# Kernel tuning notes

Measured on AMD Instinct MI355X. Metric: run time of the kernel, lower is better.

The kernel has to match this reference:

```python
import jax, jax.numpy as jnp
import numpy as np

REG = 1e-6

def maxpool2(x):  # NCHW, kernel 2 stride 2
    return jax.lax.reduce_window(x, -jnp.inf, jax.lax.max, (1, 1, 2, 2), (1, 1, 2, 2), 'VALID')

def conv2d_same(x, w, b):  # NCHW / OIHW, stride 1, padding 1 (3x3)
    y = jax.lax.conv_general_dilated(x, w, (1, 1), ((1, 1), (1, 1)),
                                     dimension_numbers=('NCHW', 'OIHW', 'NCHW'))
    return y + b[None, :, None, None]

def batch_skew(a):  # [B,3] -> [B,3,3]
    z = jnp.zeros_like(a[:, 0])
    return jnp.stack([
        jnp.stack([z, -a[:, 2], a[:, 1]], -1),
        jnp.stack([a[:, 2], z, -a[:, 0]], -1),
        jnp.stack([-a[:, 1], a[:, 0], z], -1)], 1)

def batch_twist2mat(w):  # Rodrigues: so(3) -> SO(3)
    theta = jnp.maximum(jnp.linalg.norm(w, axis=1, keepdims=True), 1e-12)  # [B,1]
    A = batch_skew(w / theta)
    s = jnp.sin(theta)[:, :, None]
    c = (1.0 - jnp.cos(theta))[:, :, None]
    return jnp.eye(3, dtype=w.dtype) + s * A + c * (A @ A)

def setup_inputs() -> dict:
    key = jax.random.key(0)
    ks = jax.random.split(key, 24)
    B, C, H, W = 64, 8, 240, 320
    HW = H * W
    A = jax.random.normal(ks[0], (B, 6, 6), jnp.float32)
    JtJ = A @ jnp.swapaxes(A, 1, 2) + 6.0 * jnp.eye(6, dtype=jnp.float32)  # SPD Hessian
    inp = {
        'JtJ': JtJ,
        'Jt': jax.random.normal(ks[1], (B, 6, HW), jnp.float32),
        'weights': jax.random.uniform(ks[2], (B, 1, H, W), jnp.float32),
        'R': jax.random.normal(ks[3], (B, 1, H, W), jnp.float32),
        'pose_R': jax.random.normal(ks[4], (B, 3, 3), jnp.float32),
        'pose_t': jax.random.normal(ks[5], (B, 3, 1), jnp.float32),
        'invD0': jax.random.uniform(ks[6], (B, 1, H, W), jnp.float32),
        'invD1': jax.random.uniform(ks[7], (B, 1, H, W), jnp.float32),
        'x0': jax.random.normal(ks[8], (B, C, H, W), jnp.float32),
        'x1': jax.random.normal(ks[9], (B, C, H, W), jnp.float32),
        'K': jax.random.normal(ks[10], (B, 3, 3), jnp.float32),
        # DampingNet parameters
        'consts': jax.random.normal(ks[11], (6, 6), jnp.float32),
        'conv1_w': jax.random.normal(ks[12], (8, 1, 3, 3), jnp.float32) * 0.2,
        'conv1_b': jnp.zeros((8,), jnp.float32),
        'conv2_w': jax.random.normal(ks[13], (16, 8, 3, 3), jnp.float32) * 0.1,
        'conv2_b': jnp.zeros((16,), jnp.float32),
        'fc1_w': jax.random.normal(ks[14], (64, 19200), jnp.float32) * 0.01,
        'fc1_b': jnp.zeros((64,), jnp.float32),
        'fc2_w': jax.random.normal(ks[15], (6, 64), jnp.float32) * 0.1,
        'fc2_b': jnp.zeros((6,), jnp.float32),
    }
    return inp

def dampingnet(R, consts, c1w, c1b, c2w, c2b, f1w, f1b, f2w, f2b):
    B = R.shape[0]
    h = maxpool2(R)
    h = jax.nn.relu(conv2d_same(h, c1w, c1b))
    h = maxpool2(h)
    h = jax.nn.relu(conv2d_same(h, c2w, c2b))
    h = maxpool2(h)
    h = h.reshape(B, -1)  # [B, 19200], NCHW flatten matches torch
    h = jax.nn.relu(h @ f1w.T + f1b)
    lambdas_w = jax.nn.softmax(h @ f2w.T + f2b, axis=-1)  # [B,6]
    wc = lambdas_w @ consts  # [B,6]
    min_, max_ = -6.0, -5.0
    return 10.0 ** (min_ + jax.nn.sigmoid(wc) * (max_ - min_))  # [B,6]

def reference(JtJ, Jt, weights, R, pose_R, pose_t, invD0, invD1, x0, x1, K,
              consts, conv1_w, conv1_b, conv2_w, conv2_b, fc1_w, fc1_b, fc2_w, fc2_b):
    B = JtJ.shape[0]
    wR = (weights * R).reshape(B, -1, 1)            # [B,HW,1]
    JtR = Jt @ wR                                   # [B,6,1]
    lam = dampingnet(R, consts, conv1_w, conv1_b, conv2_w, conv2_b,
                     fc1_w, fc1_b, fc2_w, fc2_b)    # [B,6]
    trace = jnp.trace(JtJ, axis1=1, axis2=2)        # [B]
    diag_add = lam + 1e-6 * trace[:, None]          # [B,6]
    eye6 = jnp.eye(6, dtype=JtJ.dtype)
    Hessian = JtJ + diag_add[:, :, None] * eye6     # diag_mask*lambda + epsilon
    # inverse_update_pose: regularized batched 6x6 inverse
    Hinv = jnp.linalg.inv(Hessian + REG * eye6)
    xi = Hinv @ JtR                                 # [B,6,1]
    d_R = batch_twist2mat(-xi[:, :3, 0])            # [B,3,3]
    d_t = -(d_R @ xi[:, 3:])                        # [B,3,1]
    R_new = pose_R @ d_R
    t_new = pose_R @ d_t + pose_t
    return jnp.concatenate([R_new, t_new], axis=2)  # [B,3,4] pose (R|t)
```

## Files before the change

### kernel.cpp

```cpp
#include <hip/hip_runtime.h>
#include <math.h>

#define BATCH 64
#define WW 320
#define HWTOT 76800
#define HW4 19200
#define NJTRB 512
#define JSL4 2400
#define NCONV1 1280
#define KS 64
#define NSLICE 300

__global__ __launch_bounds__(256) void k_front(
    const float* __restrict__ Jt, const float* __restrict__ wgt,
    const float* __restrict__ Rin, const float* __restrict__ c1w,
    const float* __restrict__ c1b, float* __restrict__ part,
    float* __restrict__ h1) {
  __shared__ float smem[34 * 37 + 96];
  int tid = threadIdx.x;
  if (blockIdx.x < NJTRB) {
    int b = blockIdx.x >> 3, s = blockIdx.x & 7;
    const float4* w4 = (const float4*)(wgt + (size_t)b * HWTOT);
    const float4* r4 = (const float4*)(Rin + (size_t)b * HWTOT);
    const float4* j4 = (const float4*)(Jt + (size_t)b * 6 * HWTOT);
    int base = s * JSL4;
    float acc[6] = {0.f, 0.f, 0.f, 0.f, 0.f, 0.f};
#pragma unroll 3
    for (int k = 0; k < 9; ++k) {
      int t = base + k * 256 + tid;
      float4 wv = w4[t], rv = r4[t];
      float4 p;
      p.x = wv.x * rv.x; p.y = wv.y * rv.y; p.z = wv.z * rv.z; p.w = wv.w * rv.w;
#pragma unroll
      for (int i = 0; i < 6; ++i) {
        float4 jv = j4[i * HW4 + t];
        acc[i] += jv.x * p.x + jv.y * p.y + jv.z * p.z + jv.w * p.w;
      }
    }
    if (tid < 96) {
      int t = base + 2304 + tid;
      float4 wv = w4[t], rv = r4[t];
      float4 p;
      p.x = wv.x * rv.x; p.y = wv.y * rv.y; p.z = wv.z * rv.z; p.w = wv.w * rv.w;
#pragma unroll
      for (int i = 0; i < 6; ++i) {
        float4 jv = j4[i * HW4 + t];
        acc[i] += jv.x * p.x + jv.y * p.y + jv.z * p.z + jv.w * p.w;
      }
    }
#pragma unroll
    for (int i = 0; i < 6; ++i) {
      float v = acc[i];
      for (int off = 32; off; off >>= 1) v += __shfl_down(v, off, 64);
      acc[i] = v;
    }
    float* sred = smem;
    int lane = tid & 63, wid = tid >> 6;
    if (lane == 0) {
#pragma unroll
      for (int i = 0; i < 6; ++i) sred[wid * 6 + i] = acc[i];
    }
    __syncthreads();
    if (tid < 6) {
      part[blockIdx.x * 6 + tid] =
          sred[0 + tid] + sred[6 + tid] + sred[12 + tid] + sred[18 + tid];
    }
    return;
  }
  int cb = blockIdx.x - NJTRB;
  int b = cb / 20, rem = cb % 20;
  int by = rem / 5, bx = rem % 5;
  float (*sA)[37] = (float(*)[37])smem;
  float* sW = smem + 34 * 37;
  float* sB = sW + 72;
  if (tid < 72) sW[tid] = c1w[(tid & 7) * 9 + (tid >> 3)];
  if (tid < 8) sB[tid] = c1b[tid];
  int iy0 = 32 * by - 1;
  const float* src = Rin + (size_t)b * HWTOT;
  for (int idx = tid; idx < 34 * 18; idx += 256) {
    int pr = idx / 18, c4 = idx % 18;
    int py = iy0 + pr;
    int gx = 64 * bx - 4 + 4 * c4;
    float cell0 = 0.f, cell1 = 0.f;
    if (py >= 0 && py < 120 && gx >= 0 && gx < 320) {
      const float4* row0 = (const float4*)(src + (size_t)(2 * py) * WW + gx);
      const float4* row1 = (const float4*)(src + (size_t)(2 * py + 1) * WW + gx);
      float4 v0 = row0[0], v1 = row1[0];
      cell0 = fmaxf(fmaxf(v0.x, v0.y), fmaxf(v1.x, v1.y));
      cell1 = fmaxf(fmaxf(v0.z, v0.w), fmaxf(v1.z, v1.w));
    }
    sA[pr][2 * c4] = cell0;
    sA[pr][2 * c4 + 1] = cell1;
  }
  __syncthreads();
  int ly = tid / 16, lx = tid % 16;
  int y = 16 * by + ly, x = 16 * bx + lx;
  float win[16];
#pragma unroll
  for (int r = 0; r < 4; ++r)
#pragma unroll
    for (int c = 0; c < 4; ++c) win[r * 4 + c] = sA[2 * ly + r][2 * lx + c + 1];
  float acc[8][4];
#pragma unroll
  for (int oc = 0; oc < 8; ++oc)
#pragma unroll
    for (int p = 0; p < 4; ++p) acc[oc][p] = 0.f;
#pragma unroll
  for (int tap = 0; tap < 9; ++tap) {
    int ky = tap / 3, kx = tap % 3;
#pragma unroll
    for (int oc = 0; oc < 8; ++oc) {
      float wv = sW[tap * 8 + oc];
#pragma unroll
      for (int py = 0; py < 2; ++py)
#pragma unroll
        for (int px = 0; px < 2; ++px)
          acc[oc][py * 2 + px] += wv * win[(py + ky) * 4 + (px + kx)];
    }
  }
  if (y < 60) {
    float v[8];
#pragma unroll
    for (int oc = 0; oc < 8; ++oc)
      v[oc] = fmaxf(fmaxf(fmaxf(acc[oc][0], acc[oc][1]), fmaxf(acc[oc][2], acc[oc][3])) + sB[oc], 0.f);
    float4* dst = (float4*)(h1 + (((size_t)b * 60 + y) * 80 + x) * 8);
    dst[0] = make_float4(v[0], v[1], v[2], v[3]);
    dst[1] = make_float4(v[4], v[5], v[6], v[7]);
  }
}

__global__ __launch_bounds__(256) void k_conv2(
    const float* __restrict__ h1, const float* __restrict__ c2w,
    const float* __restrict__ c2b, float* __restrict__ h2) {
  __shared__ float sA[8][34][38];
  int b = blockIdx.z >> 1, ocg = blockIdx.z & 1;
  int ty0 = blockIdx.y * 16, tx0 = blockIdx.x * 16;
  int tid = threadIdx.x;
  int iy0 = ty0 * 2 - 1, ix0 = tx0 * 2 - 1;
  const float* src = h1 + (size_t)b * 60 * 80 * 8;
  for (int idx = tid; idx < 34 * 34; idx += 256) {
    int r = idx / 34, c = idx % 34;
    int gy = iy0 + r, gx = ix0 + c;
    float4 v0 = make_float4(0.f, 0.f, 0.f, 0.f), v1 = v0;
    if (gy >= 0 && gy < 60 && gx >= 0 && gx < 80) {
      const float4* p = (const float4*)(src + ((size_t)gy * 80 + gx) * 8);
      v0 = p[0]; v1 = p[1];
    }
    sA[0][r][c] = v0.x; sA[1][r][c] = v0.y; sA[2][r][c] = v0.z; sA[3][r][c] = v0.w;
    sA[4][r][c] = v1.x; sA[5][r][c] = v1.y; sA[6][r][c] = v1.z; sA[7][r][c] = v1.w;
  }
  __syncthreads();
  int ly = tid / 16, lx = tid % 16;
  float acc[8][4];
#pragma unroll
  for (int o = 0; o < 8; ++o)
#pragma unroll
    for (int p = 0; p < 4; ++p) acc[o][p] = 0.f;
  const float* wbase = c2w + ocg * 8 * 72;
#pragma unroll
  for (int ic = 0; ic < 8; ++ic) {
    float win[16];
#pragma unroll
    for (int r = 0; r < 4; ++r)
#pragma unroll
      for (int c = 0; c < 4; ++c) win[r * 4 + c] = sA[ic][2 * ly + r][2 * lx + c];
#pragma unroll
    for (int tap = 0; tap < 9; ++tap) {
      int ky = tap / 3, kx = tap % 3;
#pragma unroll
      for (int o = 0; o < 8; ++o) {
        float wv = wbase[o * 72 + ic * 9 + tap];
#pragma unroll
        for (int py = 0; py < 2; ++py)
#pragma unroll
          for (int px = 0; px < 2; ++px)
            acc[o][py * 2 + px] += wv * win[(py + ky) * 4 + (px + kx)];
      }
    }
  }
  int y = ty0 + ly, x = tx0 + lx;
  if (y < 30 && x < 40) {
#pragma unroll
    for (int o = 0; o < 8; ++o) {
      int oc = ocg * 8 + o;
      float m = fmaxf(fmaxf(acc[o][0], acc[o][1]), fmaxf(acc[o][2], acc[o][3])) + c2b[oc];
      h2[(((size_t)b * 16 + oc) * 30 + y) * 40 + x] = fmaxf(m, 0.f);
    }
  }
}

__global__ __launch_bounds__(256) void k_fc1_part(
    const float* __restrict__ h2, const float* __restrict__ f1w,
    float* __restrict__ fcpart) {
  __shared__ __align__(16) float sH[KS * 68];
  __shared__ __align__(16) float sWt[KS * 68];
  int sl = blockIdx.x, k0 = sl * KS;
  int tid = threadIdx.x;
  for (int idx = tid; idx < 64 * KS; idx += 256) {
    int b = idx >> 6, kk = idx & 63;
    sH[kk * 68 + b] = h2[(size_t)b * 19200 + k0 + kk];
    sWt[kk * 68 + b] = f1w[(size_t)b * 19200 + k0 + kk];
  }
  __syncthreads();
  int bq = tid & 15, jq = tid >> 4;
  int b0 = bq * 4, j0 = jq * 4;
  float acc[4][4];
#pragma unroll
  for (int i = 0; i < 4; ++i)
#pragma unroll
    for (int j = 0; j < 4; ++j) acc[i][j] = 0.f;
  for (int kk = 0; kk < KS; ++kk) {
    float4 hv = *(const float4*)&sH[kk * 68 + b0];
    float4 wv = *(const float4*)&sWt[kk * 68 + j0];
    float hb[4] = {hv.x, hv.y, hv.z, hv.w};
    float wb[4] = {wv.x, wv.y, wv.z, wv.w};
#pragma unroll
    for (int i = 0; i < 4; ++i)
#pragma unroll
      for (int j = 0; j < 4; ++j) acc[i][j] += hb[i] * wb[j];
  }
#pragma unroll
  for (int i = 0; i < 4; ++i)
#pragma unroll
    for (int j = 0; j < 4; ++j)
      fcpart[(size_t)(b0 + i) * 19200 + sl * 64 + (j0 + j)] = acc[i][j];
}

__global__ __launch_bounds__(256) void k_final(
    const float* __restrict__ fcpart, const float* __restrict__ f1b,
    const float* __restrict__ f2w, const float* __restrict__ f2b,
    const float* __restrict__ consts, const float* __restrict__ part,
    const float* __restrict__ JtJ, const float* __restrict__ poseR,
    const float* __restrict__ poseT, float* __restrict__ out) {
  __shared__ __align__(16) float sred[16 * 64];
  __shared__ float fc1v[64];
  __shared__ float sf2w[384];
  __shared__ float sf2b[8];
  __shared__ float sconst[36];
  __shared__ float lg[6];
  __shared__ float lamv[6];
  __shared__ float jtrv[6];
  int b = blockIdx.x, tid = threadIdx.x;
  for (int i = tid; i < 384; i += 256) sf2w[i] = f2w[i];
  if (tid < 6) sf2b[tid] = f2b[tid];
  if (tid < 36) sconst[tid] = consts[tid];
  {
    const float4* fp4 = (const float4*)(fcpart + (size_t)b * 19200);
    int sg = tid >> 4, j4 = tid & 15;
    float4 a = make_float4(0.f, 0.f, 0.f, 0.f);
    for (int s = sg; s < NSLICE; s += 16) {
      float4 v = fp4[s * 16 + j4];
      a.x += v.x; a.y += v.y; a.z += v.z; a.w += v.w;
    }
    ((float4*)sred)[sg * 16 + j4] = a;
  }
  if (tid >= 64 && tid < 70) {
    int i = tid - 64;
    float v = 0.f;
    for (int s = 0; s < 8; ++s) v += part[(b * 8 + s) * 6 + i];
    jtrv[i] = v;
  }
  __syncthreads();
  if (tid < 64) {
    float v = 0.f;
#pragma unroll
    for (int sg = 0; sg < 16; ++sg) v += sred[sg * 64 + tid];
    fc1v[tid] = fmaxf(v + f1b[tid], 0.f);
  }
  __syncthreads();
  if (tid < 6) {
    float v = sf2b[tid];
#pragma unroll
    for (int k = 0; k < 64; ++k) v += fc1v[k] * sf2w[tid * 64 + k];
    lg[tid] = v;
  }
  __syncthreads();
  if (tid < 6) {
    float m = lg[0];
#pragma unroll
    for (int i = 1; i < 6; ++i) m = fmaxf(m, lg[i]);
    float e[6], ssum = 0.f;
#pragma unroll
    for (int i = 0; i < 6; ++i) { e[i] = expf(lg[i] - m); ssum += e[i]; }
    float inv = 1.f / ssum;
    float wc = 0.f;
#pragma unroll
    for (int i = 0; i < 6; ++i) wc += (e[i] * inv) * sconst[i * 6 + tid];
    float sg = 1.f / (1.f + expf(-wc));
    lamv[tid] = expf((-6.f + sg) * 2.302585092994046f);
  }
  __syncthreads();
  if (tid == 0) {
    float Hm[6][6];
    const float* srcH = JtJ + b * 36;
    float tr = 0.f;
#pragma unroll
    for (int i = 0; i < 6; ++i) {
#pragma unroll
      for (int jj = 0; jj < 6; ++jj) Hm[i][jj] = srcH[i * 6 + jj];
      tr += srcH[i * 6 + i];
    }
    float rhs[6];
#pragma unroll
    for (int i = 0; i < 6; ++i) {
      rhs[i] = jtrv[i];
      Hm[i][i] += lamv[i] + 1e-6f * tr + 1e-6f;
    }
    float L[6][6];
#pragma unroll
    for (int i = 0; i < 6; ++i) {
#pragma unroll
      for (int jj = 0; jj < 6; ++jj) {
        if (jj > i) continue;
        float s = Hm[i][jj];
#pragma unroll
        for (int k = 0; k < 6; ++k)
          if (k < jj) s -= L[i][k] * L[jj][k];
        if (i == jj) L[i][jj] = sqrtf(fmaxf(s, 1e-30f));
        else L[i][jj] = s / L[jj][jj];
      }
    }
    float yv[6];
#pragma unroll
    for (int i = 0; i < 6; ++i) {
      float s = rhs[i];
#pragma unroll
      for (int k = 0; k < 6; ++k)
        if (k < i) s -= L[i][k] * yv[k];
      yv[i] = s / L[i][i];
    }
    float xi[6];
#pragma unroll
    for (int ii = 5; ii >= 0; --ii) {
      float s = yv[ii];
#pragma unroll
      for (int k = 0; k < 6; ++k)
        if (k > ii) s -= L[k][ii] * xi[k];
      xi[ii] = s / L[ii][ii];
    }
    float wx = -xi[0], wy = -xi[1], wz = -xi[2];
    float th = fmaxf(sqrtf(wx * wx + wy * wy + wz * wz), 1e-12f);
    float ux = wx / th, uy = wy / th, uz = wz / th;
    float s = sinf(th), c1 = 1.f - cosf(th);
    float Rd[3][3];
    Rd[0][0] = 1.f + c1 * (ux * ux - 1.f);
    Rd[0][1] = -s * uz + c1 * (ux * uy);
    Rd[0][2] = s * uy + c1 * (ux * uz);
    Rd[1][0] = s * uz + c1 * (uy * ux);
    Rd[1][1] = 1.f + c1 * (uy * uy - 1.f);
    Rd[1][2] = -s * ux + c1 * (uy * uz);
    Rd[2][0] = -s * uy + c1 * (uz * ux);
    Rd[2][1] = s * ux + c1 * (uz * uy);
    Rd[2][2] = 1.f + c1 * (uz * uz - 1.f);
    float dt[3];
#pragma unroll
    for (int r = 0; r < 3; ++r)
      dt[r] = -(Rd[r][0] * xi[3] + Rd[r][1] * xi[4] + Rd[r][2] * xi[5]);
    const float* pR = poseR + b * 9;
    const float* pt = poseT + b * 3;
#pragma unroll
    for (int r = 0; r < 3; ++r) {
#pragma unroll
      for (int cc = 0; cc < 3; ++cc) {
        out[b * 12 + r * 4 + cc] =
            pR[r * 3 + 0] * Rd[0][cc] + pR[r * 3 + 1] * Rd[1][cc] + pR[r * 3 + 2] * Rd[2][cc];
      }
      out[b * 12 + r * 4 + 3] =
          pR[r * 3 + 0] * dt[0] + pR[r * 3 + 1] * dt[1] + pR[r * 3 + 2] * dt[2] + pt[r];
    }
  }
}

extern "C" void kernel_launch(void* const* d_in, const int* in_sizes, int n_in,
                              void* d_out, int out_size, void* d_ws, size_t ws_size,
                              hipStream_t stream) {
  const float* JtJ = (const float*)d_in[0];
  const float* Jt = (const float*)d_in[1];
  const float* wts = (const float*)d_in[2];
  const float* Rin = (const float*)d_in[3];
  const float* poseR = (const float*)d_in[4];
  const float* poseT = (const float*)d_in[5];
  const float* consts = (const float*)d_in[11];
  const float* c1w = (const float*)d_in[12];
  const float* c1b = (const float*)d_in[13];
  const float* c2w = (const float*)d_in[14];
  const float* c2b = (const float*)d_in[15];
  const float* f1w = (const float*)d_in[16];
  const float* f1b = (const float*)d_in[17];
  const float* f2w = (const float*)d_in[18];
  const float* f2b = (const float*)d_in[19];
  float* ws = (float*)d_ws;
  float* part = ws;
  float* h1 = part + 3072;
  float* h2 = h1 + 2457600;
  float* fcpart = h2 + 1228800;
  float* out = (float*)d_out;

  k_front<<<dim3(NJTRB + NCONV1), dim3(256), 0, stream>>>(Jt, wts, Rin, c1w, c1b, part, h1);
  k_conv2<<<dim3(3, 2, BATCH * 2), dim3(256), 0, stream>>>(h1, c2w, c2b, h2);
  k_fc1_part<<<dim3(NSLICE), dim3(256), 0, stream>>>(h2, f1w, fcpart);
  k_final<<<dim3(64), dim3(256), 0, stream>>>(fcpart, f1b, f2w, f2b, consts, part,
                                              JtJ, poseR, poseT, out);
}
```

Baseline: 72.10 us.

## Store conv1 activations as fp16 pairs and use fdot2 in conv2

The conv1 output h1 is now written as packed half2 values, which halves its global footprint and the shared-memory staging in conv2. Conv2's weights are packed into half2 pairs once by a block in k_front and staged into shared memory. The inner conv2 loop then uses the fdot2 instruction to handle two input channels per operation instead of scalar fp32 FMAs. This trades activation and weight precision for less memory traffic and fewer ALU instructions.

```diff
diff --git a/kernel.cpp b/kernel.cpp
--- a/kernel.cpp
+++ b/kernel.cpp
@@ -11,11 +11,34 @@
 #define KS 64
 #define NSLICE 300
 
+typedef _Float16 half2_t __attribute__((ext_vector_type(2)));
+union U32H2 { unsigned int u; half2_t h; };
+__device__ __forceinline__ unsigned int pack_h2(float a, float b) {
+  U32H2 x; x.h = half2_t{(_Float16)a, (_Float16)b}; return x.u;
+}
+__device__ __forceinline__ half2_t u_as_h2(unsigned int u) { U32H2 x; x.u = u; return x.h; }
+
+#if defined(__has_builtin)
+#if __has_builtin(__builtin_amdgcn_fdot2)
+#define HAVE_FDOT2 1
+#endif
+#endif
+
+__device__ __forceinline__ float dot2acc(unsigned int a, unsigned int b, float c) {
+#ifdef HAVE_FDOT2
+  return __builtin_amdgcn_fdot2(u_as_h2(a), u_as_h2(b), c, false);
+#else
+  half2_t ah = u_as_h2(a), bh = u_as_h2(b);
+  return c + (float)ah.x * (float)bh.x + (float)ah.y * (float)bh.y;
+#endif
+}
+
 __global__ __launch_bounds__(256) void k_front(
     const float* __restrict__ Jt, const float* __restrict__ wgt,
     const float* __restrict__ Rin, const float* __restrict__ c1w,
-    const float* __restrict__ c1b, float* __restrict__ part,
-    float* __restrict__ h1) {
+    const float* __restrict__ c1b, const float* __restrict__ c2w,
+    float* __restrict__ part, unsigned int* __restrict__ h1u,
+    unsigned int* __restrict__ wpk) {
   __shared__ float smem[34 * 37 + 96];
   int tid = threadIdx.x;
   if (blockIdx.x < NJTRB) {
@@ -70,6 +93,14 @@
   int cb = blockIdx.x - NJTRB;
   int b = cb / 20, rem = cb % 20;
   int by = rem / 5, bx = rem % 5;
+  if (cb == 0) {
+    for (int i = tid; i < 576; i += 256) {
+      int icp = i / 144, tap = (i % 144) / 16, oc = i % 16;
+      float lo = c2w[oc * 72 + (2 * icp) * 9 + tap];
+      float hi = c2w[oc * 72 + (2 * icp + 1) * 9 + tap];
+      wpk[i] = pack_h2(lo, hi);
+    }
+  }
   float (*sA)[37] = (float(*)[37])smem;
   float* sW = smem + 34 * 37;
   float* sB = sW + 72;
@@ -123,31 +154,36 @@
 #pragma unroll
     for (int oc = 0; oc < 8; ++oc)
       v[oc] = fmaxf(fmaxf(fmaxf(acc[oc][0], acc[oc][1]), fmaxf(acc[oc][2], acc[oc][3])) + sB[oc], 0.f);
-    float4* dst = (float4*)(h1 + (((size_t)b * 60 + y) * 80 + x) * 8);
-    dst[0] = make_float4(v[0], v[1], v[2], v[3]);
-    dst[1] = make_float4(v[4], v[5], v[6], v[7]);
+    uint4 st;
+    st.x = pack_h2(v[0], v[1]);
+    st.y = pack_h2(v[2], v[3]);
+    st.z = pack_h2(v[4], v[5]);
+    st.w = pack_h2(v[6], v[7]);
+    *(uint4*)(h1u + (((size_t)b * 60 + y) * 80 + x) * 4) = st;
   }
 }
 
 __global__ __launch_bounds__(256) void k_conv2(
-    const float* __restrict__ h1, const float* __restrict__ c2w,
+    const unsigned int* __restrict__ h1u, const unsigned int* __restrict__ wpk,
     const float* __restrict__ c2b, float* __restrict__ h2) {
-  __shared__ float sA[8][34][38];
+  __shared__ unsigned int sA[4][34][38];
+  __shared__ __align__(16) unsigned int sW[288];
   int b = blockIdx.z >> 1, ocg = blockIdx.z & 1;
   int ty0 = blockIdx.y * 16, tx0 = blockIdx.x * 16;
   int tid = threadIdx.x;
+  for (int i = tid; i < 288; i += 256) {
+    int icp = i / 72, tap = (i % 72) / 8, o = i % 8;
+    sW[i] = wpk[icp * 144 + tap * 16 + ocg * 8 + o];
+  }
   int iy0 = ty0 * 2 - 1, ix0 = tx0 * 2 - 1;
-  const float* src = h1 + (size_t)b * 60 * 80 * 8;
+  const unsigned int* src = h1u + (size_t)b * 60 * 80 * 4;
   for (int idx = tid; idx < 34 * 34; idx += 256) {
     int r = idx / 34, c = idx % 34;
     int gy = iy0 + r, gx = ix0 + c;
-    float4 v0 = make_float4(0.f, 0.f, 0.f, 0.f), v1 = v0;
-    if (gy >= 0 && gy < 60 && gx >= 0 && gx < 80) {
-      const float4* p = (const float4*)(src + ((size_t)gy * 80 + gx) * 8);
-      v0 = p[0]; v1 = p[1];
-    }
-    sA[0][r][c] = v0.x; sA[1][r][c] = v0.y; sA[2][r][c] = v0.z; sA[3][r][c] = v0.w;
-    sA[4][r][c] = v1.x; sA[5][r][c] = v1.y; sA[6][r][c] = v1.z; sA[7][r][c] = v1.w;
+    uint4 v = make_uint4(0u, 0u, 0u, 0u);
+    if (gy >= 0 && gy < 60 && gx >= 0 && gx < 80)
+      v = *(const uint4*)(src + ((size_t)gy * 80 + gx) * 4);
+    sA[0][r][c] = v.x; sA[1][r][c] = v.y; sA[2][r][c] = v.z; sA[3][r][c] = v.w;
   }
   __syncthreads();
   int ly = tid / 16, lx = tid % 16;
@@ -156,25 +192,28 @@
   for (int o = 0; o < 8; ++o)
 #pragma unroll
     for (int p = 0; p < 4; ++p) acc[o][p] = 0.f;
-  const float* wbase = c2w + ocg * 8 * 72;
-#pragma unroll
-  for (int ic = 0; ic < 8; ++ic) {
-    float win[16];
+  const uint4* sW4 = (const uint4*)sW;
+#pragma unroll
+  for (int icp = 0; icp < 4; ++icp) {
+    unsigned int win[16];
 #pragma unroll
     for (int r = 0; r < 4; ++r)
 #pragma unroll
-      for (int c = 0; c < 4; ++c) win[r * 4 + c] = sA[ic][2 * ly + r][2 * lx + c];
+      for (int c = 0; c < 4; ++c) win[r * 4 + c] = sA[icp][2 * ly + r][2 * lx + c];
 #pragma unroll
     for (int tap = 0; tap < 9; ++tap) {
       int ky = tap / 3, kx = tap % 3;
+      uint4 wa = sW4[(icp * 9 + tap) * 2];
+      uint4 wb = sW4[(icp * 9 + tap) * 2 + 1];
+      unsigned int warr[8] = {wa.x, wa.y, wa.z, wa.w, wb.x, wb.y, wb.z, wb.w};
 #pragma unroll
       for (int o = 0; o < 8; ++o) {
-        float wv = wbase[o * 72 + ic * 9 + tap];
 #pragma unroll
         for (int py = 0; py < 2; ++py)
 #pragma unroll
           for (int px = 0; px < 2; ++px)
-            acc[o][py * 2 + px] += wv * win[(py + ky) * 4 + (px + kx)];
+            acc[o][py * 2 + px] =
+                dot2acc(win[(py + ky) * 4 + (px + kx)], warr[o], acc[o][py * 2 + px]);
       }
     }
   }
@@ -391,13 +430,15 @@
   const float* f2b = (const float*)d_in[19];
   float* ws = (float*)d_ws;
   float* part = ws;
-  float* h1 = part + 3072;
-  float* h2 = h1 + 2457600;
+  unsigned int* h1u = (unsigned int*)(ws + 3072);
+  float* h2 = ws + 3072 + 1228800;
   float* fcpart = h2 + 1228800;
+  unsigned int* wpk = (unsigned int*)(fcpart + 1228800);
   float* out = (float*)d_out;
 
-  k_front<<<dim3(NJTRB + NCONV1), dim3(256), 0, stream>>>(Jt, wts, Rin, c1w, c1b, part, h1);
-  k_conv2<<<dim3(3, 2, BATCH * 2), dim3(256), 0, stream>>>(h1, c2w, c2b, h2);
+  k_front<<<dim3(NJTRB + NCONV1), dim3(256), 0, stream>>>(Jt, wts, Rin, c1w, c1b, c2w,
+                                                          part, h1u, wpk);
+  k_conv2<<<dim3(3, 2, BATCH * 2), dim3(256), 0, stream>>>(h1u, wpk, c2b, h2);
   k_fc1_part<<<dim3(NSLICE), dim3(256), 0, stream>>>(h2, f1w, fcpart);
   k_final<<<dim3(64), dim3(256), 0, stream>>>(fcpart, f1b, f2w, f2b, consts, part,
                                               JtJ, poseR, poseT, out);
```

Result: faster. 67.47 us (-6.4%).
